# Performance work log

Measured on AMD Instinct MI355X. Metric: run time of the kernel, lower is better.

The kernel has to match this reference:

```python
import jax, jax.numpy as jnp
import numpy as np

B, L, D = 4, 512, 128

def setup_inputs() -> dict:
    key = jax.random.key(0)
    k1, k2, k3, k4 = jax.random.split(key, 4)
    s = 1.0 / np.sqrt(D)
    return {
        "inp": jax.random.normal(k1, (B, L, D), dtype=jnp.float32),
        "Wu": jax.random.normal(k2, (D, D), dtype=jnp.float32) * s,
        "Ww": jax.random.normal(k3, (D, D), dtype=jnp.float32) * s,
        "Wv": jax.random.normal(k4, (1, D), dtype=jnp.float32) * s,
    }

def reference(inp, Wu, Ww, Wv):
    # inp: (B,L,D); torch Linear weights are (out,in), so y = x @ W.T
    qu = inp @ Wu.T                      # (B,L,D), u(inp)
    kw = inp @ Ww.T                      # (B,L,D), w(inp)
    # qu.unsqueeze(1) -> broadcast over i; kw.unsqueeze(2) -> broadcast over j
    # h[b,i,j,:] = tanh(u(inp)[b,j] + w(inp)[b,i])   (dropout = identity in eval)
    h = jnp.tanh(qu[:, None, :, :] + kw[:, :, None, :])   # (B,L,L,D)
    score = jnp.einsum('bijd,d->bij', h, Wv[0])           # (B,L,L)
    attn = jax.nn.softmax(score, axis=2)                  # softmax over keys j
    out = jnp.einsum('bij,bjd->bid', attn, inp)           # bmm(attn, inp)
    return out, attn
```

## Files before the change

### kernel.cpp

```cpp
#include <hip/hip_runtime.h>

#define BD 128
#define SL 512
#define NB 4

__device__ __forceinline__ float rcp_fast(float x) { return __builtin_amdgcn_rcpf(x); }

__global__ __launch_bounds__(256, 2) void k_qk(const float* __restrict__ inp,
                                               const float* __restrict__ Wu,
                                               const float* __restrict__ Ww,
                                               float* __restrict__ Equ,
                                               float* __restrict__ Ekw) {
    __shared__ float sx[4][BD];
    __shared__ float swT[2][32][BD + 1];

    const int t  = threadIdx.x;
    const int r0 = blockIdx.x * 4;
    const int b  = r0 >> 9;
    const int l0 = r0 & (SL - 1);

    #pragma unroll
    for (int h = 0; h < 2; ++h) {
        int idx = h * 256 + t;
        sx[idx >> 7][idx & 127] = inp[(size_t)(r0 + (idx >> 7)) * BD + (idx & 127)];
    }

    const int m = t >> 7, o = t & 127;
    float acc[4] = {0.f, 0.f, 0.f, 0.f};

    for (int k0 = 0; k0 < BD; k0 += 32) {
        __syncthreads();
        #pragma unroll
        for (int i = 0; i < 32; ++i) {
            int idx = i * 256 + t;
            int mm  = idx >> 12;
            int rem = idx & 4095;
            int oo  = rem >> 5, kk = rem & 31;
            swT[mm][kk][oo] = (mm ? Ww : Wu)[oo * BD + k0 + kk];
        }
        __syncthreads();
        #pragma unroll
        for (int kk = 0; kk < 32; kk += 4) {
            float w0 = swT[m][kk + 0][o];
            float w1 = swT[m][kk + 1][o];
            float w2 = swT[m][kk + 2][o];
            float w3 = swT[m][kk + 3][o];
            #pragma unroll
            for (int rr = 0; rr < 4; ++rr) {
                float4 x = *(const float4*)&sx[rr][k0 + kk];
                acc[rr] = fmaf(x.x, w0, acc[rr]);
                acc[rr] = fmaf(x.y, w1, acc[rr]);
                acc[rr] = fmaf(x.z, w2, acc[rr]);
                acc[rr] = fmaf(x.w, w3, acc[rr]);
            }
        }
    }

    if (m == 0) {
        #pragma unroll
        for (int rr = 0; rr < 4; ++rr)
            Equ[((size_t)b * BD + o) * SL + l0 + rr] = __expf(2.f * acc[rr]);
    } else {
        #pragma unroll
        for (int rr = 0; rr < 4; ++rr)
            Ekw[(size_t)(r0 + rr) * BD + o] = __expf(2.f * acc[rr]);
    }
}

__global__ __launch_bounds__(256, 2) void k_attn(const float* __restrict__ inp,
                                                 const float* __restrict__ Wv,
                                                 const float* __restrict__ Equ,
                                                 const float* __restrict__ Ekw,
                                                 float* __restrict__ out,
                                                 float* __restrict__ attn) {
    __shared__ float4 s_ce[BD];
    __shared__ float  s_wv[BD];
    __shared__ float4 s_p[SL];
    __shared__ float  s_fin[4][4][BD];
    __shared__ float  s_red[4][4];

    const int t  = threadIdx.x;
    const int b  = blockIdx.x >> 7;
    const int i0 = (blockIdx.x & 127) * 4;

    if (t < BD) {
        const float* ek = Ekw + ((size_t)b * SL + i0) * BD + t;
        s_ce[t] = make_float4(ek[0], ek[BD], ek[2 * BD], ek[3 * BD]);
        s_wv[t] = Wv[t];
    }
    __syncthreads();

    const float2* equ2 = (const float2*)(Equ + (size_t)b * BD * SL);
    float a[4][2];
    #pragma unroll
    for (int i = 0; i < 4; ++i) { a[i][0] = 0.f; a[i][1] = 0.f; }

    #pragma unroll 4
    for (int d = 0; d < BD; ++d) {
        float2 q = equ2[d * (SL / 2) + t];
        float4 e = s_ce[d];
        float  w = s_wv[d];
        a[0][0] = fmaf(w, rcp_fast(fmaf(q.x, e.x, 1.f)), a[0][0]);
        a[0][1] = fmaf(w, rcp_fast(fmaf(q.y, e.x, 1.f)), a[0][1]);
        a[1][0] = fmaf(w, rcp_fast(fmaf(q.x, e.y, 1.f)), a[1][0]);
        a[1][1] = fmaf(w, rcp_fast(fmaf(q.y, e.y, 1.f)), a[1][1]);
        a[2][0] = fmaf(w, rcp_fast(fmaf(q.x, e.z, 1.f)), a[2][0]);
        a[2][1] = fmaf(w, rcp_fast(fmaf(q.y, e.z, 1.f)), a[2][1]);
        a[3][0] = fmaf(w, rcp_fast(fmaf(q.x, e.w, 1.f)), a[3][0]);
        a[3][1] = fmaf(w, rcp_fast(fmaf(q.y, e.w, 1.f)), a[3][1]);
    }

    const int wid = t >> 6;
    float mn[4];
    #pragma unroll
    for (int i = 0; i < 4; ++i) mn[i] = fminf(a[i][0], a[i][1]);
    #pragma unroll
    for (int off = 32; off > 0; off >>= 1) {
        #pragma unroll
        for (int i = 0; i < 4; ++i) mn[i] = fminf(mn[i], __shfl_xor(mn[i], off, 64));
    }
    if ((t & 63) == 0) {
        #pragma unroll
        for (int i = 0; i < 4; ++i) s_red[i][wid] = mn[i];
    }
    __syncthreads();
    #pragma unroll
    for (int i = 0; i < 4; ++i)
        mn[i] = fminf(fminf(s_red[i][0], s_red[i][1]), fminf(s_red[i][2], s_red[i][3]));

    float p[4][2], sm[4];
    #pragma unroll
    for (int i = 0; i < 4; ++i) {
        p[i][0] = __expf(-2.f * (a[i][0] - mn[i]));
        p[i][1] = __expf(-2.f * (a[i][1] - mn[i]));
        sm[i]   = p[i][0] + p[i][1];
    }
    #pragma unroll
    for (int off = 32; off > 0; off >>= 1) {
        #pragma unroll
        for (int i = 0; i < 4; ++i) sm[i] += __shfl_xor(sm[i], off, 64);
    }
    __syncthreads();
    if ((t & 63) == 0) {
        #pragma unroll
        for (int i = 0; i < 4; ++i) s_red[i][wid] = sm[i];
    }
    __syncthreads();
    float rs[4];
    #pragma unroll
    for (int i = 0; i < 4; ++i)
        rs[i] = rcp_fast(s_red[i][0] + s_red[i][1] + s_red[i][2] + s_red[i][3]);

    float n0[4], n1[4];
    #pragma unroll
    for (int i = 0; i < 4; ++i) { n0[i] = p[i][0] * rs[i]; n1[i] = p[i][1] * rs[i]; }
    #pragma unroll
    for (int i = 0; i < 4; ++i) {
        float2* at = (float2*)(attn + ((size_t)b * SL + i0 + i) * SL);
        at[t] = make_float2(n0[i], n1[i]);
    }
    s_p[2 * t]     = make_float4(n0[0], n0[1], n0[2], n0[3]);
    s_p[2 * t + 1] = make_float4(n1[0], n1[1], n1[2], n1[3]);
    __syncthreads();

    const int dv = t & 63, jh = t >> 6;
    const float2* inp2 = (const float2*)(inp + (size_t)b * SL * BD);
    float o0[4] = {0.f, 0.f, 0.f, 0.f}, o1[4] = {0.f, 0.f, 0.f, 0.f};
    #pragma unroll 4
    for (int jj = 0; jj < SL / 4; ++jj) {
        int j = jh * (SL / 4) + jj;
        float2 x  = inp2[j * (BD / 2) + dv];
        float4 p4 = s_p[j];
        o0[0] = fmaf(p4.x, x.x, o0[0]);  o1[0] = fmaf(p4.x, x.y, o1[0]);
        o0[1] = fmaf(p4.y, x.x, o0[1]);  o1[1] = fmaf(p4.y, x.y, o1[1]);
        o0[2] = fmaf(p4.z, x.x, o0[2]);  o1[2] = fmaf(p4.z, x.y, o1[2]);
        o0[3] = fmaf(p4.w, x.x, o0[3]);  o1[3] = fmaf(p4.w, x.y, o1[3]);
    }
    #pragma unroll
    for (int i = 0; i < 4; ++i) {
        s_fin[jh][i][2 * dv]     = o0[i];
        s_fin[jh][i][2 * dv + 1] = o1[i];
    }
    __syncthreads();
    #pragma unroll
    for (int h = 0; h < 2; ++h) {
        int id = h * 256 + t;
        int i = id >> 7, d = id & 127;
        float s = s_fin[0][i][d] + s_fin[1][i][d] + s_fin[2][i][d] + s_fin[3][i][d];
        out[((size_t)b * SL + i0 + i) * BD + d] = s;
    }
}

extern "C" void kernel_launch(void* const* d_in, const int* in_sizes, int n_in,
                              void* d_out, int out_size, void* d_ws, size_t ws_size,
                              hipStream_t stream) {
    const float* inp = (const float*)d_in[0];
    const float* Wu  = (const float*)d_in[1];
    const float* Ww  = (const float*)d_in[2];
    const float* Wv  = (const float*)d_in[3];

    float* out  = (float*)d_out;
    float* attn = out + (size_t)NB * SL * BD;

    float* ws  = (float*)d_ws;
    float* Equ = ws;
    float* Ekw = Equ + (size_t)NB * BD * SL;

    k_qk<<<NB * SL / 4, 256, 0, stream>>>(inp, Wu, Ww, Equ, Ekw);
    k_attn<<<NB * SL / 4, 256, 0, stream>>>(inp, Wv, Equ, Ekw, out, attn);
}
```

Before: 100.3 us.

## Retile attention kernel to eight query rows per 512-thread block

The attention kernel now handles eight query rows per block with 512 threads, one key per thread, instead of four rows with two keys per thread. The query-side exp values are staged in shared memory laid out for float4 reads. The output bmm is restructured so each wavefront owns one query row, which removes the cross-wave partial-sum reduction through shared memory. The aim is to halve global reloads of Equ and inp per output row, at the cost of fewer blocks (256) and more registers per thread.

```diff
diff --git a/kernel.cpp b/kernel.cpp
--- a/kernel.cpp
+++ b/kernel.cpp
@@ -67,128 +67,115 @@
     }
 }
 
-__global__ __launch_bounds__(256, 2) void k_attn(const float* __restrict__ inp,
+__global__ __launch_bounds__(512, 2) void k_attn(const float* __restrict__ inp,
                                                  const float* __restrict__ Wv,
                                                  const float* __restrict__ Equ,
                                                  const float* __restrict__ Ekw,
                                                  float* __restrict__ out,
                                                  float* __restrict__ attn) {
-    __shared__ float4 s_ce[BD];
-    __shared__ float  s_wv[BD];
-    __shared__ float4 s_p[SL];
-    __shared__ float  s_fin[4][4][BD];
-    __shared__ float  s_red[4][4];
+    __shared__ float s_ek[BD][8];
+    __shared__ float s_wv[BD];
+    __shared__ float s_p[8][SL];
+    __shared__ float s_red[8][8];
 
     const int t  = threadIdx.x;
-    const int b  = blockIdx.x >> 7;
-    const int i0 = (blockIdx.x & 127) * 4;
+    const int b  = blockIdx.x >> 6;
+    const int i0 = (blockIdx.x & 63) * 8;
 
-    if (t < BD) {
-        const float* ek = Ekw + ((size_t)b * SL + i0) * BD + t;
-        s_ce[t] = make_float4(ek[0], ek[BD], ek[2 * BD], ek[3 * BD]);
-        s_wv[t] = Wv[t];
+    #pragma unroll
+    for (int h = 0; h < 2; ++h) {
+        int id = h * 512 + t;
+        int i = id >> 7, d = id & 127;
+        s_ek[d][i] = Ekw[((size_t)b * SL + i0 + i) * BD + d];
     }
+    if (t < BD) s_wv[t] = Wv[t];
     __syncthreads();
 
-    const float2* equ2 = (const float2*)(Equ + (size_t)b * BD * SL);
-    float a[4][2];
+    const float* equ = Equ + (size_t)b * BD * SL;
+    float a[8];
     #pragma unroll
-    for (int i = 0; i < 4; ++i) { a[i][0] = 0.f; a[i][1] = 0.f; }
+    for (int i = 0; i < 8; ++i) a[i] = 0.f;
 
     #pragma unroll 4
     for (int d = 0; d < BD; ++d) {
-        float2 q = equ2[d * (SL / 2) + t];
-        float4 e = s_ce[d];
-        float  w = s_wv[d];
-        a[0][0] = fmaf(w, rcp_fast(fmaf(q.x, e.x, 1.f)), a[0][0]);
-        a[0][1] = fmaf(w, rcp_fast(fmaf(q.y, e.x, 1.f)), a[0][1]);
-        a[1][0] = fmaf(w, rcp_fast(fmaf(q.x, e.y, 1.f)), a[1][0]);
-        a[1][1] = fmaf(w, rcp_fast(fmaf(q.y, e.y, 1.f)), a[1][1]);
-        a[2][0] = fmaf(w, rcp_fast(fmaf(q.x, e.z, 1.f)), a[2][0]);
-        a[2][1] = fmaf(w, rcp_fast(fmaf(q.y, e.z, 1.f)), a[2][1]);
-        a[3][0] = fmaf(w, rcp_fast(fmaf(q.x, e.w, 1.f)), a[3][0]);
-        a[3][1] = fmaf(w, rcp_fast(fmaf(q.y, e.w, 1.f)), a[3][1]);
+        float  q  = equ[d * SL + t];
+        float4 e0 = *(const float4*)&s_ek[d][0];
+        float4 e1 = *(const float4*)&s_ek[d][4];
+        float  w  = s_wv[d];
+        a[0] = fmaf(w, rcp_fast(fmaf(q, e0.x, 1.f)), a[0]);
+        a[1] = fmaf(w, rcp_fast(fmaf(q, e0.y, 1.f)), a[1]);
+        a[2] = fmaf(w, rcp_fast(fmaf(q, e0.z, 1.f)), a[2]);
+        a[3] = fmaf(w, rcp_fast(fmaf(q, e0.w, 1.f)), a[3]);
+        a[4] = fmaf(w, rcp_fast(fmaf(q, e1.x, 1.f)), a[4]);
+        a[5] = fmaf(w, rcp_fast(fmaf(q, e1.y, 1.f)), a[5]);
+        a[6] = fmaf(w, rcp_fast(fmaf(q, e1.z, 1.f)), a[6]);
+        a[7] = fmaf(w, rcp_fast(fmaf(q, e1.w, 1.f)), a[7]);
     }
 
     const int wid = t >> 6;
-    float mn[4];
+    float mn[8];
     #pragma unroll
-    for (int i = 0; i < 4; ++i) mn[i] = fminf(a[i][0], a[i][1]);
+    for (int i = 0; i < 8; ++i) mn[i] = a[i];
     #pragma unroll
     for (int off = 32; off > 0; off >>= 1) {
         #pragma unroll
-        for (int i = 0; i < 4; ++i) mn[i] = fminf(mn[i], __shfl_xor(mn[i], off, 64));
+        for (int i = 0; i < 8; ++i) mn[i] = fminf(mn[i], __shfl_xor(mn[i], off, 64));
     }
     if ((t & 63) == 0) {
         #pragma unroll
-        for (int i = 0; i < 4; ++i) s_red[i][wid] = mn[i];
+        for (int i = 0; i < 8; ++i) s_red[i][wid] = mn[i];
     }
     __syncthreads();
     #pragma unroll
-    for (int i = 0; i < 4; ++i)
-        mn[i] = fminf(fminf(s_red[i][0], s_red[i][1]), fminf(s_red[i][2], s_red[i][3]));
+    for (int i = 0; i < 8; ++i) {
+        float4 r0 = *(const float4*)&s_red[i][0];
+        float4 r1 = *(const float4*)&s_red[i][4];
+        mn[i] = fminf(fminf(fminf(r0.x, r0.y), fminf(r0.z, r0.w)),
+                      fminf(fminf(r1.x, r1.y), fminf(r1.z, r1.w)));
+    }
 
-    float p[4][2], sm[4];
+    float p[8], sm[8];
     #pragma unroll
-    for (int i = 0; i < 4; ++i) {
-        p[i][0] = __expf(-2.f * (a[i][0] - mn[i]));
-        p[i][1] = __expf(-2.f * (a[i][1] - mn[i]));
-        sm[i]   = p[i][0] + p[i][1];
-    }
+    for (int i = 0; i < 8; ++i) { p[i] = __expf(-2.f * (a[i] - mn[i])); sm[i] = p[i]; }
     #pragma unroll
     for (int off = 32; off > 0; off >>= 1) {
         #pragma unroll
-        for (int i = 0; i < 4; ++i) sm[i] += __shfl_xor(sm[i], off, 64);
+        for (int i = 0; i < 8; ++i) sm[i] += __shfl_xor(sm[i], off, 64);
     }
     __syncthreads();
     if ((t & 63) == 0) {
         #pragma unroll
-        for (int i = 0; i < 4; ++i) s_red[i][wid] = sm[i];
-    }
-    __syncthreads();
-    float rs[4];
-    #pragma unroll
-    for (int i = 0; i < 4; ++i)
-        rs[i] = rcp_fast(s_red[i][0] + s_red[i][1] + s_red[i][2] + s_red[i][3]);
-
-    float n0[4], n1[4];
-    #pragma unroll
-    for (int i = 0; i < 4; ++i) { n0[i] = p[i][0] * rs[i]; n1[i] = p[i][1] * rs[i]; }
-    #pragma unroll
-    for (int i = 0; i < 4; ++i) {
-        float2* at = (float2*)(attn + ((size_t)b * SL + i0 + i) * SL);
-        at[t] = make_float2(n0[i], n1[i]);
-    }
-    s_p[2 * t]     = make_float4(n0[0], n0[1], n0[2], n0[3]);
-    s_p[2 * t + 1] = make_float4(n1[0], n1[1], n1[2], n1[3]);
-    __syncthreads();
-
-    const int dv = t & 63, jh = t >> 6;
-    const float2* inp2 = (const float2*)(inp + (size_t)b * SL * BD);
-    float o0[4] = {0.f, 0.f, 0.f, 0.f}, o1[4] = {0.f, 0.f, 0.f, 0.f};
-    #pragma unroll 4
-    for (int jj = 0; jj < SL / 4; ++jj) {
-        int j = jh * (SL / 4) + jj;
-        float2 x  = inp2[j * (BD / 2) + dv];
-        float4 p4 = s_p[j];
-        o0[0] = fmaf(p4.x, x.x, o0[0]);  o1[0] = fmaf(p4.x, x.y, o1[0]);
-        o0[1] = fmaf(p4.y, x.x, o0[1]);  o1[1] = fmaf(p4.y, x.y, o1[1]);
-        o0[2] = fmaf(p4.z, x.x, o0[2]);  o1[2] = fmaf(p4.z, x.y, o1[2]);
-        o0[3] = fmaf(p4.w, x.x, o0[3]);  o1[3] = fmaf(p4.w, x.y, o1[3]);
-    }
-    #pragma unroll
-    for (int i = 0; i < 4; ++i) {
-        s_fin[jh][i][2 * dv]     = o0[i];
-        s_fin[jh][i][2 * dv + 1] = o1[i];
+        for (int i = 0; i < 8; ++i) s_red[i][wid] = sm[i];
     }
     __syncthreads();
     #pragma unroll
-    for (int h = 0; h < 2; ++h) {
-        int id = h * 256 + t;
-        int i = id >> 7, d = id & 127;
-        float s = s_fin[0][i][d] + s_fin[1][i][d] + s_fin[2][i][d] + s_fin[3][i][d];
-        out[((size_t)b * SL + i0 + i) * BD + d] = s;
+    for (int i = 0; i < 8; ++i) {
+        float4 r0 = *(const float4*)&s_red[i][0];
+        float4 r1 = *(const float4*)&s_red[i][4];
+        float rs = rcp_fast((r0.x + r0.y) + (r0.z + r0.w) + (r1.x + r1.y) + (r1.z + r1.w));
+        float n  = p[i] * rs;
+        attn[((size_t)b * SL + i0 + i) * SL + t] = n;
+        s_p[i][t] = n;
     }
+    __syncthreads();
+
+    const int d2 = t & 63, ig = t >> 6;
+    const float2* inp2 = (const float2*)(inp + (size_t)b * SL * BD);
+    float o0 = 0.f, o1 = 0.f;
+    #pragma unroll 2
+    for (int j4 = 0; j4 < SL / 4; ++j4) {
+        float4 p4 = *(const float4*)&s_p[ig][j4 * 4];
+        float2 x0 = inp2[(j4 * 4 + 0) * (BD / 2) + d2];
+        float2 x1 = inp2[(j4 * 4 + 1) * (BD / 2) + d2];
+        float2 x2 = inp2[(j4 * 4 + 2) * (BD / 2) + d2];
+        float2 x3 = inp2[(j4 * 4 + 3) * (BD / 2) + d2];
+        o0 = fmaf(p4.x, x0.x, o0);  o1 = fmaf(p4.x, x0.y, o1);
+        o0 = fmaf(p4.y, x1.x, o0);  o1 = fmaf(p4.y, x1.y, o1);
+        o0 = fmaf(p4.z, x2.x, o0);  o1 = fmaf(p4.z, x2.y, o1);
+        o0 = fmaf(p4.w, x3.x, o0);  o1 = fmaf(p4.w, x3.y, o1);
+    }
+    float2* outp = (float2*)(out + ((size_t)b * SL + i0 + ig) * BD);
+    outp[d2] = make_float2(o0, o1);
 }
 
 extern "C" void kernel_launch(void* const* d_in, const int* in_sizes, int n_in,
@@ -207,5 +194,5 @@
     float* Ekw = Equ + (size_t)NB * BD * SL;
 
     k_qk<<<NB * SL / 4, 256, 0, stream>>>(inp, Wu, Ww, Equ, Ekw);
-    k_attn<<<NB * SL / 4, 256, 0, stream>>>(inp, Wv, Equ, Ekw, out, attn);
+    k_attn<<<NB * SL / 8, 512, 0, stream>>>(inp, Wv, Equ, Ekw, out, attn);
 }
```

Result: slower. 121.0 us (+20.6%).
